# Kernel optimization log

Hardware: AMD Instinct MI355X
Metric: run time of the kernel (lower is better)

## Reference

```python
import jax, jax.numpy as jnp
import numpy as np

N, E, S, K, NB = 16384, 262144, 10, 64, 8
R_MAX, P_CUT, AVG_NEIGH = 5.0, 5, 16.0
L_OF_LM = np.array([0, 1, 1, 1, 2, 2, 2, 2, 2])  # l value of each of the 9 lm components
L_SLICES = [(0, 1), (1, 4), (4, 9)]               # lm ranges for l = 0,1,2
MLP_H = 16


def _sph(u):
    # real spherical harmonics up to l=2, e3nn 'component' normalization (sum_m Y_lm^2 = 2l+1)
    x, y, z = u[..., 0], u[..., 1], u[..., 2]
    s3, s15, s5 = np.float32(np.sqrt(3.0)), np.float32(np.sqrt(15.0)), np.float32(np.sqrt(5.0))
    return jnp.stack([
        jnp.ones_like(x),
        s3 * x, s3 * y, s3 * z,
        s15 * x * y, s15 * y * z, (s5 / 2) * (3 * z * z - 1), s15 * x * z, (s15 / 2) * (x * x - y * y),
    ], axis=-1)


def _radial(r):
    # Bessel radial basis with smooth polynomial cutoff envelope (p = P_CUT)
    u = r / R_MAX
    r_safe = jnp.where(r > 1e-9, r, 1.0)
    n = jnp.arange(1, NB + 1, dtype=r.dtype)
    bess = np.float32(np.sqrt(2.0 / R_MAX)) * jnp.sin(n * jnp.pi * u[:, None]) / r_safe[:, None]
    p = float(P_CUT)
    env = 1.0 - (p + 1) * (p + 2) / 2 * u**P_CUT + p * (p + 2) * u**(P_CUT + 1) - p * (p + 1) / 2 * u**(P_CUT + 2)
    env = jnp.where(u < 1.0, env, 0.0)
    return bess * env[:, None]  # [E, NB]


def setup_inputs() -> dict:
    key = jax.random.key(0)
    ks = jax.random.split(key, 16)
    positions = jax.random.uniform(ks[0], (N, 3), jnp.float32) * 4.0  # box so many edges fall inside r_max
    species = jax.random.randint(ks[1], (N,), 0, S)
    senders = jax.random.randint(ks[2], (E,), 0, N)
    receivers = jax.random.randint(ks[3], (E,), 0, N)
    shifts = jnp.zeros((E, 3), jnp.float32)
    W_embed = jax.random.normal(ks[4], (S, K), jnp.float32)
    W_rad = jax.random.normal(ks[5], (2, 3, NB, K), jnp.float32) * 0.3
    W_mix = jax.random.normal(ks[6], (2, 3, K, K), jnp.float32) / np.sqrt(K)
    W_prod = jax.random.normal(ks[7], (2, 3, 3, K), jnp.float32) * 0.1
    W_sc = jax.random.normal(ks[8], (2, S, 3, K, K), jnp.float32) / np.sqrt(K)
    W_ro0 = jax.random.normal(ks[9], (K,), jnp.float32) / np.sqrt(K)
    W_m1 = jax.random.normal(ks[10], (K, MLP_H), jnp.float32) / np.sqrt(K)
    b_m1 = jnp.zeros((MLP_H,), jnp.float32)
    W_m2 = jax.random.normal(ks[11], (MLP_H,), jnp.float32) / np.sqrt(MLP_H)
    return dict(positions=positions, shifts=shifts, species=species, senders=senders,
                receivers=receivers, W_embed=W_embed, W_rad=W_rad, W_mix=W_mix,
                W_prod=W_prod, W_sc=W_sc, W_ro0=W_ro0, W_m1=W_m1, b_m1=b_m1, W_m2=W_m2)


def reference(positions, shifts, species, senders, receivers, W_embed, W_rad, W_mix,
              W_prod, W_sc, W_ro0, W_m1, b_m1, W_m2):
    lm = jnp.asarray(L_OF_LM)
    onehot = jax.nn.one_hot(species, S, dtype=positions.dtype)
    # node embedding: scalars only -> feats [N, 9(lm), K]
    feats = jnp.zeros((N, 9, K), positions.dtype).at[:, 0, :].set(onehot @ W_embed)

    # edge geometry
    vec = positions[receivers] - positions[senders] + shifts           # [E, 3]
    r = jnp.linalg.norm(vec, axis=-1)                                  # [E]
    u_hat = vec / jnp.where(r > 1e-9, r, 1.0)[:, None]
    Y = _sph(u_hat)                                                     # [E, 9]
    rad = _radial(r)                                                    # [E, NB]

    energies = []
    for i in range(2):
        # interaction: radial-weighted SH messages from sender scalars, scatter-sum to receivers
        hs = feats[:, 0, :][senders]                                    # [E, K]
        Rl = jnp.einsum('eb,lbk->elk', rad, W_rad[i])[:, lm, :]         # [E, 9, K]
        msg = hs[:, None, :] * Y[:, :, None] * Rl                       # [E, 9, K]
        A = jax.ops.segment_sum(msg, receivers, num_segments=N) / AVG_NEIGH
        A = jnp.einsum('nmk,mkj->nmj', A, W_mix[i][lm])                 # per-l channel mixing

        # correlation-3 equivariant product basis (symmetric-contraction style)
        A0 = A[:, 0, :]
        inv = jnp.sum(A * A, axis=1)                                    # rotation-invariant [N, K]
        w1, w2, w3 = (W_prod[i, j][lm] for j in range(3))               # each [9, K]
        B = A * (w1[None] + w2[None] * A0[:, None, :] + w3[None] * inv[:, None, :])

        # species-dependent self-connection (linear of feats x node_attrs), per-l weights
        sc = jnp.concatenate([
            jnp.einsum('nmk,ns,skj->nmj', feats[:, st:en], onehot, W_sc[i, :, l])
            for l, (st, en) in enumerate(L_SLICES)], axis=1)
        feats = B + sc

        if i == 0:
            energies.append(feats[:, 0, :] @ W_ro0)                     # linear readout
        else:
            feats = feats.at[:, 1:, :].set(0.0)                         # last layer keeps 0e only
            energies.append(jax.nn.silu(feats[:, 0, :] @ W_m1 + b_m1) @ W_m2)

    return jnp.stack(energies, axis=1)  # [N, num_interactions]
```

## Files before the change

kernel.cpp:

```cpp
#include <hip/hip_runtime.h>

#define NN 16384
#define NE 262144
#define NSPEC 10
#define KC 64
#define MLPH 16
#define SEG 128
#define EPSG 2048

__device__ __forceinline__ float wave_reduce(float v) {
#pragma unroll
    for (int off = 32; off > 0; off >>= 1) v += __shfl_down(v, off, 64);
    return v;
}

__device__ __forceinline__ float f4c(const float4& v, int j) {
    const float* p = &v.x;
    return p[j];
}

__global__ void __launch_bounds__(1024) k_pre(
    const float* __restrict__ W_embed,
    const int* __restrict__ species,
    const int* __restrict__ receivers,
    int* __restrict__ eslot,
    unsigned short* __restrict__ cnt16,
    float4* __restrict__ h04) {
    __shared__ int cntL[NN];
    int t = threadIdx.x;
#pragma unroll
    for (int i = 0; i < 16; ++i) cntL[t + 1024 * i] = 0;
    __syncthreads();
    int ebase = blockIdx.x * EPSG;
#pragma unroll
    for (int j = 0; j < EPSG / 1024; ++j) {
        int e = ebase + j * 1024 + t;
        int r = receivers[e];
        eslot[e] = atomicAdd(&cntL[r], 1);
    }
    int gt = blockIdx.x * 1024 + t;
#pragma unroll
    for (int q = 0; q < 2; ++q) {
        int idx = gt * 2 + q;
        int n = idx >> 4, w = idx & 15;
        h04[idx] = reinterpret_cast<const float4*>(W_embed + species[n] * KC)[w];
    }
    __syncthreads();
    unsigned short* o = cnt16 + (size_t)blockIdx.x * NN;
#pragma unroll
    for (int i = 0; i < 16; ++i)
        o[t + 1024 * i] = (unsigned short)cntL[t + 1024 * i];
}

__global__ void __launch_bounds__(128) k_colscan(
    const unsigned short* __restrict__ cnt16,
    int* __restrict__ seg_base,
    int* __restrict__ count) {
    int r = blockIdx.x * 128 + threadIdx.x;
    int run = 0;
#pragma unroll 4
    for (int g = 0; g < SEG; ++g) {
        int c = cnt16[(size_t)g * NN + r];
        seg_base[(size_t)g * NN + r] = run;
        run += c;
    }
    count[r] = run;
}

__global__ void __launch_bounds__(1024) k_scan(
    const int* __restrict__ count, int* __restrict__ row_start,
    const int* __restrict__ species, int* __restrict__ nslot,
    int* __restrict__ sp_start) {
    __shared__ int lds[1024];
    __shared__ int itercnt[256 * NSPEC];
    __shared__ int spt[NSPEC];
    int t = threadIdx.x;
    int lane = t & 63;
    int w = t >> 6;
#pragma unroll
    for (int j = 0; j < 16; ++j) {
        int n = w * 1024 + j * 64 + lane;
        int sp = species[n];
#pragma unroll
        for (int s = 0; s < NSPEC; ++s) {
            unsigned long long mask = __ballot(sp == s);
            if (lane == 0) itercnt[(w * 16 + j) * NSPEC + s] = (int)__popcll(mask);
        }
    }
    int base = t * 16;
    int local[16];
    int ssum = 0;
#pragma unroll
    for (int b = 0; b < 16; ++b) { local[b] = count[base + b]; ssum += local[b]; }
    lds[t] = ssum;
    __syncthreads();
    for (int off = 1; off < 1024; off <<= 1) {
        int v = (t >= off) ? lds[t - off] : 0;
        __syncthreads();
        lds[t] += v;
        __syncthreads();
    }
    int run = lds[t] - ssum;
#pragma unroll
    for (int b = 0; b < 16; ++b) { row_start[base + b] = run; run += local[b]; }
    if (t == 1023) row_start[NN] = run;
    __syncthreads();
    if (t < NSPEC) {
        int r2 = 0;
        for (int i = 0; i < 256; ++i) {
            int v = itercnt[i * NSPEC + t];
            itercnt[i * NSPEC + t] = r2;
            r2 += v;
        }
        spt[t] = r2;
    }
    __syncthreads();
    if (t == 0) {
        int r2 = 0;
        for (int s = 0; s < NSPEC; ++s) { sp_start[s] = r2; r2 += spt[s]; }
        sp_start[NSPEC] = r2;
    }
#pragma unroll
    for (int j = 0; j < 16; ++j) {
        int n = w * 1024 + j * 64 + lane;
        int sp = species[n];
        int rank = 0;
#pragma unroll
        for (int s = 0; s < NSPEC; ++s) {
            unsigned long long mask = __ballot(sp == s);
            if (sp == s)
                rank = (int)__popcll(mask & ((1ull << lane) - 1ull));
        }
        nslot[n] = itercnt[(w * 16 + j) * NSPEC + sp] + rank;
    }
}

__global__ void k_geom(const float* __restrict__ pos,
                       const float* __restrict__ shifts,
                       const int* __restrict__ senders,
                       const int* __restrict__ receivers,
                       const int* __restrict__ row_start,
                       const int* __restrict__ seg_base,
                       const int* __restrict__ eslot,
                       const int* __restrict__ species,
                       const int* __restrict__ sp_start,
                       const int* __restrict__ nslot,
                       int* __restrict__ ord,
                       float* __restrict__ edgerec,
                       int* __restrict__ ssend) {
    int e = blockIdx.x * 256 + threadIdx.x;
    if (e < NN) {
        int sp = species[e];
        ord[sp_start[sp] + nslot[e]] = e;
    }
    int s = senders[e], r = receivers[e];
    float dx = pos[r * 3 + 0] - pos[s * 3 + 0] + shifts[e * 3 + 0];
    float dy = pos[r * 3 + 1] - pos[s * 3 + 1] + shifts[e * 3 + 1];
    float dz = pos[r * 3 + 2] - pos[s * 3 + 2] + shifts[e * 3 + 2];
    float rn = sqrtf(dx * dx + dy * dy + dz * dz);
    float den = (rn > 1e-9f) ? rn : 1.0f;
    float x = dx / den, y = dy / den, z = dz / den;
    const float s3  = 1.7320508075688772f;
    const float s15 = 3.8729833462074170f;
    const float s5h = 1.1180339887498949f;
    const float s15h = 1.9364916731037085f;
    float rec[16];
    rec[0] = s3 * x;
    rec[1] = s3 * y;
    rec[2] = s3 * z;
    rec[3] = s15 * x * y;
    rec[4] = s15 * y * z;
    rec[5] = s5h * (3.0f * z * z - 1.0f);
    rec[6] = s15 * x * z;
    rec[7] = s15h * (x * x - y * y);
    float u = rn * 0.2f;
    float env = 0.0f;
    if (u < 1.0f) {
        float u2 = u * u;
        float u5 = u2 * u2 * u;
        env = 1.0f - 21.0f * u5 + 35.0f * u5 * u - 15.0f * u5 * u2;
    }
    float pre = 0.63245553203367587f * env / den;
#pragma unroll
    for (int nb = 1; nb <= 8; ++nb)
        rec[7 + nb] = pre * sinf((float)nb * 3.14159265358979323846f * u);
    int p = row_start[r] + seg_base[(size_t)(e >> 11) * NN + r] + eslot[e];
    float4* o = (float4*)(edgerec + (size_t)p * 16);
#pragma unroll
    for (int i = 0; i < 4; ++i)
        o[i] = make_float4(rec[4 * i], rec[4 * i + 1], rec[4 * i + 2], rec[4 * i + 3]);
    ssend[p] = s;
}

__device__ __forceinline__ void agg_edge(const float* __restrict__ rec, float hv,
                                         const float (&Wr)[3][8], float (&acc)[9]) {
    float R0 = 0.f, R1 = 0.f, R2 = 0.f;
#pragma unroll
    for (int b = 0; b < 8; ++b) {
        float rb = rec[8 + b];
        R0 += rb * Wr[0][b];
        R1 += rb * Wr[1][b];
        R2 += rb * Wr[2][b];
    }
    float t0 = hv * R0, t1 = hv * R1, t2 = hv * R2;
    acc[0] += t0;
    acc[1] += t1 * rec[0];
    acc[2] += t1 * rec[1];
    acc[3] += t1 * rec[2];
    acc[4] += t2 * rec[3];
    acc[5] += t2 * rec[4];
    acc[6] += t2 * rec[5];
    acc[7] += t2 * rec[6];
    acc[8] += t2 * rec[7];
}

#define AMX_NPW 2
__global__ void __launch_bounds__(512, 6) k_aggmix(
    const float* __restrict__ h,
    const float* __restrict__ edgerec,
    const int* __restrict__ ssend,
    const int* __restrict__ row_start,
    const float* __restrict__ Wr_i,
    const float* __restrict__ Wm_i,
    const float* __restrict__ Wp_i,
    float* __restrict__ Bm0) {
    __shared__ float Wlds[2 * 4096];
    __shared__ float xtile[8][9 * 64];
    {
        float4* Wl4 = (float4*)Wlds;
        const float4* W4 = (const float4*)(Wm_i + 4096);
#pragma unroll
        for (int i = 0; i < 4; ++i)
            Wl4[threadIdx.x + 512 * i] = W4[threadIdx.x + 512 * i];
    }
    __syncthreads();
    int lane = threadIdx.x & 63;
    int wid = __builtin_amdgcn_readfirstlane(threadIdx.x >> 6);
    float* xt = xtile[wid];
    float Wr[3][8];
#pragma unroll
    for (int l = 0; l < 3; ++l)
#pragma unroll
        for (int b = 0; b < 8; ++b)
            Wr[l][b] = Wr_i[(l * 8 + b) * 64 + lane] * (1.0f / 16.0f);
    float w10 = Wp_i[0 * 64 + lane];
    float w20 = Wp_i[3 * 64 + lane];
    float w30 = Wp_i[6 * 64 + lane];
    const float* W0g = Wm_i;
    int n0 = (blockIdx.x * 8 + wid) * AMX_NPW;
    for (int it = 0; it < AMX_NPW; ++it) {
        int n = n0 + it;
        float acc[9];
#pragma unroll
        for (int m = 0; m < 9; ++m) acc[m] = 0.f;
        int e0 = row_start[n], e1 = row_start[n + 1];
#pragma unroll 4
        for (int e = e0; e < e1; ++e) {
            int s = ssend[e];
            float hv = h[(size_t)s * 64 + lane];
            const float* rc = edgerec + (size_t)e * 16;
            agg_edge(rc, hv, Wr, acc);
        }
#pragma unroll
        for (int m = 0; m < 9; ++m) xt[m * 64 + lane] = acc[m];
        float mix[9];
#pragma unroll
        for (int m = 0; m < 9; ++m) mix[m] = 0.f;
#pragma unroll 2
        for (int c4 = 0; c4 < 16; ++c4) {
            float4 xb[9];
#pragma unroll
            for (int m = 0; m < 9; ++m)
                xb[m] = *(const float4*)&xt[m * 64 + c4 * 4];
#pragma unroll
            for (int j = 0; j < 4; ++j) {
                int k = c4 * 4 + j;
                float wv0 = W0g[k * 64 + lane];
                float wv1 = Wlds[k * 64 + lane];
                float wv2 = Wlds[4096 + k * 64 + lane];
                mix[0] += f4c(xb[0], j) * wv0;
                mix[1] += f4c(xb[1], j) * wv1;
                mix[2] += f4c(xb[2], j) * wv1;
                mix[3] += f4c(xb[3], j) * wv1;
                mix[4] += f4c(xb[4], j) * wv2;
                mix[5] += f4c(xb[5], j) * wv2;
                mix[6] += f4c(xb[6], j) * wv2;
                mix[7] += f4c(xb[7], j) * wv2;
                mix[8] += f4c(xb[8], j) * wv2;
            }
        }
        float A0 = mix[0];
        float inv = 0.f;
#pragma unroll
        for (int m = 0; m < 9; ++m) inv += mix[m] * mix[m];
        Bm0[(size_t)n * 64 + lane] = mix[0] * (w10 + w20 * A0 + w30 * inv);
    }
}

#define RPB 32
template <int ITER>
__global__ void __launch_bounds__(256) k_sc(
    const float* __restrict__ h_in,
    const float* __restrict__ Bm0,
    float* __restrict__ h_out,
    const int* __restrict__ ord,
    const int* __restrict__ sp_start,
    const float* __restrict__ Wsc_i,
    const float* __restrict__ W_ro0,
    const float* __restrict__ W_m1,
    const float* __restrict__ b_m1,
    const float* __restrict__ W_m2,
    float* __restrict__ out) {
    const int BPS = NN / RPB;
    int sp = blockIdx.x / BPS;
    int c  = blockIdx.x - sp * BPS;
    int base = sp_start[sp];
    int cnt  = sp_start[sp + 1] - base;
    int r0 = c * RPB;
    __shared__ float Wlds[4096];
    __shared__ float xtile[4][8 * 64];
    if (r0 < cnt) {
        const float4* W4 = (const float4*)(Wsc_i + (size_t)sp * 3 * 4096);
        float4* Wl4 = (float4*)Wlds;
#pragma unroll
        for (int i = 0; i < 4; ++i)
            Wl4[threadIdx.x + 256 * i] = W4[threadIdx.x + 256 * i];
    }
    __syncthreads();
    if (r0 >= cnt) return;
    int lane = threadIdx.x & 63;
    int wid = threadIdx.x >> 6;
    float* xt = xtile[wid];
    int rend = min(r0 + RPB, cnt);
    int q0 = r0 + wid * 8;
    if (q0 >= rend) return;
    int nd[8];
#pragma unroll
    for (int t = 0; t < 8; ++t)
        nd[t] = ord[base + min(q0 + t, rend - 1)];
    float xv[8];
#pragma unroll
    for (int t = 0; t < 8; ++t) xv[t] = h_in[(size_t)nd[t] * 64 + lane];
#pragma unroll
    for (int t = 0; t < 8; ++t) xt[t * 64 + lane] = xv[t];
    float acc[8];
#pragma unroll
    for (int t = 0; t < 8; ++t) acc[t] = 0.f;
#pragma unroll 2
    for (int c4 = 0; c4 < 16; ++c4) {
        float wv[4];
#pragma unroll
        for (int j = 0; j < 4; ++j) wv[j] = Wlds[(c4 * 4 + j) * 64 + lane];
#pragma unroll
        for (int t = 0; t < 8; ++t) {
            float4 xb = *(const float4*)&xt[t * 64 + c4 * 4];
#pragma unroll
            for (int j = 0; j < 4; ++j) acc[t] += f4c(xb, j) * wv[j];
        }
    }
    float wro = W_ro0[lane];
#pragma unroll
    for (int t = 0; t < 8; ++t) {
        if (q0 + t >= rend) break;
        int node = nd[t];
        float outv = acc[t] + Bm0[(size_t)node * 64 + lane];
        if (ITER == 0) {
            h_out[(size_t)node * 64 + lane] = outv;
            float e = wave_reduce(outv * wro);
            if (lane == 0) out[2 * node + 0] = e;
        } else {
            int hh = lane & 15;
            float tacc = b_m1[hh];
#pragma unroll
            for (int k = 0; k < 64; ++k)
                tacc += __shfl(outv, k, 64) * W_m1[k * MLPH + hh];
            float sig = 1.0f / (1.0f + expf(-tacc));
            float contrib = (lane < MLPH) ? tacc * sig * W_m2[lane] : 0.f;
            float e = wave_reduce(contrib);
            if (lane == 0) out[2 * node + 1] = e;
        }
    }
}

extern "C" void kernel_launch(void* const* d_in, const int* in_sizes, int n_in,
                              void* d_out, int out_size, void* d_ws, size_t ws_size,
                              hipStream_t stream) {
    const float* positions = (const float*)d_in[0];
    const float* shifts    = (const float*)d_in[1];
    const int*   species   = (const int*)d_in[2];
    const int*   senders   = (const int*)d_in[3];
    const int*   receivers = (const int*)d_in[4];
    const float* W_embed   = (const float*)d_in[5];
    const float* W_rad     = (const float*)d_in[6];
    const float* W_mix     = (const float*)d_in[7];
    const float* W_prod    = (const float*)d_in[8];
    const float* W_sc      = (const float*)d_in[9];
    const float* W_ro0     = (const float*)d_in[10];
    const float* W_m1      = (const float*)d_in[11];
    const float* b_m1      = (const float*)d_in[12];
    const float* W_m2      = (const float*)d_in[13];
    float* out = (float*)d_out;

    char* p = (char*)d_ws;
    float* edgerec = (float*)p; p += (size_t)NE * 16 * 4;
    int* seg_base  = (int*)p;   p += (size_t)SEG * NN * 4;
    float* Bm0     = (float*)p; p += (size_t)NN * KC * 4;
    float* h0      = (float*)p; p += (size_t)NN * KC * 4;
    float* h1      = (float*)p; p += (size_t)NN * KC * 4;
    unsigned short* cnt16 = (unsigned short*)p; p += (size_t)SEG * NN * 2;
    int* eslot     = (int*)p; p += (size_t)NE * 4;
    int* ssend     = (int*)p; p += (size_t)NE * 4;
    int* nslot     = (int*)p; p += (size_t)NN * 4;
    int* ord       = (int*)p; p += (size_t)NN * 4;
    int* count     = (int*)p; p += (size_t)NN * 4;
    int* row_start = (int*)p; p += (size_t)(NN + 1) * 4;
    int* sp_start  = (int*)p; p += 16 * 4;

    k_pre<<<SEG, 1024, 0, stream>>>(W_embed, species, receivers,
                                    eslot, cnt16, (float4*)h0);
    k_colscan<<<NN / 128, 128, 0, stream>>>(cnt16, seg_base, count);
    k_scan<<<1, 1024, 0, stream>>>(count, row_start, species, nslot, sp_start);
    k_geom<<<NE / 256, 256, 0, stream>>>(positions, shifts, senders, receivers,
                                         row_start, seg_base, eslot, species,
                                         sp_start, nslot, ord, edgerec, ssend);

    k_aggmix<<<NN / (8 * AMX_NPW), 512, 0, stream>>>(h0, edgerec, ssend, row_start,
        W_rad + 0, W_mix + 0, W_prod + 0, Bm0);
    k_sc<0><<<NSPEC * (NN / RPB), 256, 0, stream>>>(h0, Bm0, h1, ord, sp_start,
        W_sc + 0, W_ro0, W_m1, b_m1, W_m2, out);

    k_aggmix<<<NN / (8 * AMX_NPW), 512, 0, stream>>>(h1, edgerec, ssend, row_start,
        W_rad + 1536, W_mix + 12288, W_prod + 576, Bm0);
    k_sc<1><<<NSPEC * (NN / RPB), 256, 0, stream>>>(h1, Bm0, h0 , ord,
        sp_start, W_sc + (size_t)NSPEC * 3 * 4096, W_ro0, W_m1, b_m1, W_m2, out);
}
```

Baseline: 295.6 us.

## Parallelize scans with wave shuffles, use packed FMA and hardware sin

```diff
diff --git a/kernel.cpp b/kernel.cpp
--- a/kernel.cpp
+++ b/kernel.cpp
@@ -7,6 +7,8 @@
 #define MLPH 16
 #define SEG 128
 #define EPSG 2048
+
+typedef float v2f __attribute__((ext_vector_type(2)));
 
 __device__ __forceinline__ float wave_reduce(float v) {
 #pragma unroll
@@ -52,19 +54,25 @@
         o[t + 1024 * i] = (unsigned short)cntL[t + 1024 * i];
 }
 
-__global__ void __launch_bounds__(128) k_colscan(
+__global__ void __launch_bounds__(256) k_colscan(
     const unsigned short* __restrict__ cnt16,
     int* __restrict__ seg_base,
     int* __restrict__ count) {
-    int r = blockIdx.x * 128 + threadIdx.x;
-    int run = 0;
-#pragma unroll 4
-    for (int g = 0; g < SEG; ++g) {
-        int c = cnt16[(size_t)g * NN + r];
-        seg_base[(size_t)g * NN + r] = run;
-        run += c;
-    }
-    count[r] = run;
+    int lane = threadIdx.x & 63;
+    int r = blockIdx.x * 4 + (threadIdx.x >> 6);
+    int c0 = cnt16[(size_t)(2 * lane) * NN + r];
+    int c1 = cnt16[(size_t)(2 * lane + 1) * NN + r];
+    int s = c0 + c1;
+    int inc = s;
+#pragma unroll
+    for (int off = 1; off < 64; off <<= 1) {
+        int v = __shfl_up(inc, off, 64);
+        if (lane >= off) inc += v;
+    }
+    int exc = inc - s;
+    seg_base[(size_t)(2 * lane) * NN + r] = exc;
+    seg_base[(size_t)(2 * lane + 1) * NN + r] = exc + c0;
+    if (lane == 63) count[r] = inc;
 }
 
 __global__ void __launch_bounds__(1024) k_scan(
@@ -105,14 +113,25 @@
     for (int b = 0; b < 16; ++b) { row_start[base + b] = run; run += local[b]; }
     if (t == 1023) row_start[NN] = run;
     __syncthreads();
-    if (t < NSPEC) {
-        int r2 = 0;
-        for (int i = 0; i < 256; ++i) {
-            int v = itercnt[i * NSPEC + t];
-            itercnt[i * NSPEC + t] = r2;
-            r2 += v;
-        }
-        spt[t] = r2;
+    if (w < NSPEC) {
+        int s = w;
+        int v0 = itercnt[(lane * 4 + 0) * NSPEC + s];
+        int v1 = itercnt[(lane * 4 + 1) * NSPEC + s];
+        int v2 = itercnt[(lane * 4 + 2) * NSPEC + s];
+        int v3 = itercnt[(lane * 4 + 3) * NSPEC + s];
+        int ls = v0 + v1 + v2 + v3;
+        int inc = ls;
+#pragma unroll
+        for (int off = 1; off < 64; off <<= 1) {
+            int v = __shfl_up(inc, off, 64);
+            if (lane >= off) inc += v;
+        }
+        int exc = inc - ls;
+        itercnt[(lane * 4 + 0) * NSPEC + s] = exc;
+        itercnt[(lane * 4 + 1) * NSPEC + s] = exc + v0;
+        itercnt[(lane * 4 + 2) * NSPEC + s] = exc + v0 + v1;
+        itercnt[(lane * 4 + 3) * NSPEC + s] = exc + v0 + v1 + v2;
+        if (lane == 63) spt[s] = inc;
     }
     __syncthreads();
     if (t == 0) {
@@ -120,6 +139,7 @@
         for (int s = 0; s < NSPEC; ++s) { sp_start[s] = r2; r2 += spt[s]; }
         sp_start[NSPEC] = r2;
     }
+    __syncthreads();
 #pragma unroll
     for (int j = 0; j < 16; ++j) {
         int n = w * 1024 + j * 64 + lane;
@@ -181,37 +201,19 @@
         env = 1.0f - 21.0f * u5 + 35.0f * u5 * u - 15.0f * u5 * u2;
     }
     float pre = 0.63245553203367587f * env / den;
-#pragma unroll
-    for (int nb = 1; nb <= 8; ++nb)
-        rec[7 + nb] = pre * sinf((float)nb * 3.14159265358979323846f * u);
+    float half_u = 0.5f * u;
+#pragma unroll
+    for (int nb = 1; nb <= 8; ++nb) {
+        float tr = (float)nb * half_u;
+        tr -= floorf(tr);
+        rec[7 + nb] = pre * __builtin_amdgcn_sinf(tr);
+    }
     int p = row_start[r] + seg_base[(size_t)(e >> 11) * NN + r] + eslot[e];
     float4* o = (float4*)(edgerec + (size_t)p * 16);
 #pragma unroll
     for (int i = 0; i < 4; ++i)
         o[i] = make_float4(rec[4 * i], rec[4 * i + 1], rec[4 * i + 2], rec[4 * i + 3]);
     ssend[p] = s;
-}
-
-__device__ __forceinline__ void agg_edge(const float* __restrict__ rec, float hv,
-                                         const float (&Wr)[3][8], float (&acc)[9]) {
-    float R0 = 0.f, R1 = 0.f, R2 = 0.f;
-#pragma unroll
-    for (int b = 0; b < 8; ++b) {
-        float rb = rec[8 + b];
-        R0 += rb * Wr[0][b];
-        R1 += rb * Wr[1][b];
-        R2 += rb * Wr[2][b];
-    }
-    float t0 = hv * R0, t1 = hv * R1, t2 = hv * R2;
-    acc[0] += t0;
-    acc[1] += t1 * rec[0];
-    acc[2] += t1 * rec[1];
-    acc[3] += t1 * rec[2];
-    acc[4] += t2 * rec[3];
-    acc[5] += t2 * rec[4];
-    acc[6] += t2 * rec[5];
-    acc[7] += t2 * rec[6];
-    acc[8] += t2 * rec[7];
 }
 
 #define AMX_NPW 2
@@ -237,12 +239,14 @@
     int lane = threadIdx.x & 63;
     int wid = __builtin_amdgcn_readfirstlane(threadIdx.x >> 6);
     float* xt = xtile[wid];
-    float Wr[3][8];
-#pragma unroll
-    for (int l = 0; l < 3; ++l)
-#pragma unroll
-        for (int b = 0; b < 8; ++b)
-            Wr[l][b] = Wr_i[(l * 8 + b) * 64 + lane] * (1.0f / 16.0f);
+    float Wr0[8];
+    v2f  Wr12[8];
+#pragma unroll
+    for (int b = 0; b < 8; ++b) {
+        Wr0[b]    = Wr_i[b * 64 + lane] * (1.0f / 16.0f);
+        Wr12[b].x = Wr_i[(8 + b) * 64 + lane] * (1.0f / 16.0f);
+        Wr12[b].y = Wr_i[(16 + b) * 64 + lane] * (1.0f / 16.0f);
+    }
     float w10 = Wp_i[0 * 64 + lane];
     float w20 = Wp_i[3 * 64 + lane];
     float w30 = Wp_i[6 * 64 + lane];
@@ -250,22 +254,39 @@
     int n0 = (blockIdx.x * 8 + wid) * AMX_NPW;
     for (int it = 0; it < AMX_NPW; ++it) {
         int n = n0 + it;
-        float acc[9];
-#pragma unroll
-        for (int m = 0; m < 9; ++m) acc[m] = 0.f;
+        float acc0 = 0.f;
+        v2f accp[4];
+#pragma unroll
+        for (int q = 0; q < 4; ++q) accp[q] = (v2f){0.f, 0.f};
         int e0 = row_start[n], e1 = row_start[n + 1];
 #pragma unroll 4
         for (int e = e0; e < e1; ++e) {
             int s = ssend[e];
             float hv = h[(size_t)s * 64 + lane];
             const float* rc = edgerec + (size_t)e * 16;
-            agg_edge(rc, hv, Wr, acc);
-        }
-#pragma unroll
-        for (int m = 0; m < 9; ++m) xt[m * 64 + lane] = acc[m];
-        float mix[9];
-#pragma unroll
-        for (int m = 0; m < 9; ++m) mix[m] = 0.f;
+            float R0 = 0.f;
+            v2f R12 = (v2f){0.f, 0.f};
+#pragma unroll
+            for (int b = 0; b < 8; ++b) {
+                float rb = rc[8 + b];
+                R0 = fmaf(rb, Wr0[b], R0);
+                R12 = __builtin_elementwise_fma((v2f){rb, rb}, Wr12[b], R12);
+            }
+            acc0 = fmaf(hv, R0, acc0);
+            float t1 = hv * R12.x, t2 = hv * R12.y;
+            accp[0] = __builtin_elementwise_fma((v2f){t1, t1}, (v2f){rc[0], rc[1]}, accp[0]);
+            accp[1] = __builtin_elementwise_fma((v2f){t1, t2}, (v2f){rc[2], rc[3]}, accp[1]);
+            accp[2] = __builtin_elementwise_fma((v2f){t2, t2}, (v2f){rc[4], rc[5]}, accp[2]);
+            accp[3] = __builtin_elementwise_fma((v2f){t2, t2}, (v2f){rc[6], rc[7]}, accp[3]);
+        }
+        xt[0 * 64 + lane] = acc0;
+        xt[1 * 64 + lane] = accp[0].x;  xt[2 * 64 + lane] = accp[0].y;
+        xt[3 * 64 + lane] = accp[1].x;  xt[4 * 64 + lane] = accp[1].y;
+        xt[5 * 64 + lane] = accp[2].x;  xt[6 * 64 + lane] = accp[2].y;
+        xt[7 * 64 + lane] = accp[3].x;  xt[8 * 64 + lane] = accp[3].y;
+        v2f mixp[9];
+#pragma unroll
+        for (int m = 0; m < 9; ++m) mixp[m] = (v2f){0.f, 0.f};
 #pragma unroll 2
         for (int c4 = 0; c4 < 16; ++c4) {
             float4 xb[9];
@@ -273,22 +294,22 @@
             for (int m = 0; m < 9; ++m)
                 xb[m] = *(const float4*)&xt[m * 64 + c4 * 4];
 #pragma unroll
-            for (int j = 0; j < 4; ++j) {
-                int k = c4 * 4 + j;
-                float wv0 = W0g[k * 64 + lane];
-                float wv1 = Wlds[k * 64 + lane];
-                float wv2 = Wlds[4096 + k * 64 + lane];
-                mix[0] += f4c(xb[0], j) * wv0;
-                mix[1] += f4c(xb[1], j) * wv1;
-                mix[2] += f4c(xb[2], j) * wv1;
-                mix[3] += f4c(xb[3], j) * wv1;
-                mix[4] += f4c(xb[4], j) * wv2;
-                mix[5] += f4c(xb[5], j) * wv2;
-                mix[6] += f4c(xb[6], j) * wv2;
-                mix[7] += f4c(xb[7], j) * wv2;
-                mix[8] += f4c(xb[8], j) * wv2;
+            for (int j2 = 0; j2 < 2; ++j2) {
+                int k0 = c4 * 4 + j2 * 2;
+                v2f wv0 = (v2f){W0g[k0 * 64 + lane], W0g[(k0 + 1) * 64 + lane]};
+                v2f wv1 = (v2f){Wlds[k0 * 64 + lane], Wlds[(k0 + 1) * 64 + lane]};
+                v2f wv2 = (v2f){Wlds[4096 + k0 * 64 + lane], Wlds[4096 + (k0 + 1) * 64 + lane]};
+#pragma unroll
+                for (int m = 0; m < 9; ++m) {
+                    v2f xp = (v2f){f4c(xb[m], j2 * 2), f4c(xb[m], j2 * 2 + 1)};
+                    v2f wv = (m == 0) ? wv0 : ((m < 4) ? wv1 : wv2);
+                    mixp[m] = __builtin_elementwise_fma(xp, wv, mixp[m]);
+                }
             }
         }
+        float mix[9];
+#pragma unroll
+        for (int m = 0; m < 9; ++m) mix[m] = mixp[m].x + mixp[m].y;
         float A0 = mix[0];
         float inv = 0.f;
 #pragma unroll
@@ -418,7 +439,7 @@
 
     k_pre<<<SEG, 1024, 0, stream>>>(W_embed, species, receivers,
                                     eslot, cnt16, (float4*)h0);
-    k_colscan<<<NN / 128, 128, 0, stream>>>(cnt16, seg_base, count);
+    k_colscan<<<NN / 4, 256, 0, stream>>>(cnt16, seg_base, count);
     k_scan<<<1, 1024, 0, stream>>>(count, row_start, species, nslot, sp_start);
     k_geom<<<NE / 256, 256, 0, stream>>>(positions, shifts, senders, receivers,
                                          row_start, seg_base, eslot, species,
```

Measured after the change: 295.2 us. About the same (-0.1%).
